# Performance work log

Measured on AMD Instinct MI355X. Metric: run time of the kernel, lower is better.

The kernel has to match this reference:

```python
import jax, jax.numpy as jnp
import numpy as np

B, T, C = 2, 2048, 2048
H, HKV, DH = 32, 8, 64
G = H // HKV  # kv_group_size = 4


def setup_inputs() -> dict:
    key = jax.random.key(0)
    k1, k2, k3, k4 = jax.random.split(key, 4)
    x = jax.random.normal(k1, (B, T, C), dtype=jnp.float32)
    Wq = jax.random.normal(k2, (C, C), dtype=jnp.float32) * 0.02
    Wkv = jax.random.normal(k3, (2 * HKV * DH, C), dtype=jnp.float32) * 0.02
    Wo = jax.random.normal(k4, (C, C), dtype=jnp.float32) * 0.02
    # RoPE tables: cos/sin of shape (T, DH/2)
    inv_freq = 1.0 / (10000.0 ** (jnp.arange(0, DH // 2, dtype=jnp.float32) / (DH // 2)))
    ang = jnp.arange(T, dtype=jnp.float32)[:, None] * inv_freq[None, :]  # (T, DH/2)
    return {"x": x, "cos": jnp.cos(ang), "sin": jnp.sin(ang), "Wq": Wq, "Wkv": Wkv, "Wo": Wo}


def _rotate_half(t):
    t1, t2 = jnp.split(t, 2, axis=-1)
    return jnp.concatenate([-t2, t1], axis=-1)


def reference(x, cos, sin, Wq, Wkv, Wo):
    # Projections (torch Linear: y = x @ W.T)
    q = (x @ Wq.T).reshape(B, T, H, DH).transpose(0, 2, 1, 3)      # (B,H,T,DH)
    kv = (x @ Wkv.T).reshape(B, T, 2, HKV, DH)
    k = kv[:, :, 0].transpose(0, 2, 1, 3)                          # (B,HKV,T,DH)
    v = kv[:, :, 1].transpose(0, 2, 1, 3)
    # RoPE
    cos2 = jnp.concatenate([cos, cos], axis=-1)[None, None]        # (1,1,T,DH)
    sin2 = jnp.concatenate([sin, sin], axis=-1)[None, None]
    q = q * cos2 + _rotate_half(q) * sin2
    k = k * cos2 + _rotate_half(k) * sin2
    # Grouped-query attention without materializing repeated K/V:
    # view q as (B, HKV, G, T, DH) and contract against shared K/V heads.
    qg = q.reshape(B, HKV, G, T, DH)
    scale = 1.0 / jnp.sqrt(jnp.float32(DH))
    scores = jnp.einsum("bhgqd,bhkd->bhgqk", qg, k) * scale        # (B,HKV,G,T,T)
    causal = jnp.tril(jnp.ones((T, T), dtype=bool))
    scores = jnp.where(causal[None, None, None], scores, -jnp.inf)
    attn = jax.nn.softmax(scores, axis=-1)
    out = jnp.einsum("bhgqk,bhkd->bhgqd", attn, v)                 # (B,HKV,G,T,DH)
    out = out.reshape(B, H, T, DH).transpose(0, 2, 1, 3).reshape(B, T, C)
    return out @ Wo.T
```

## Files before the change

kernel.cpp:

```cpp
#include <hip/hip_runtime.h>
#include <hip/hip_bf16.h>

#define B_    2
#define T_    2048
#define C_    2048
#define H_    32
#define HKV_  8
#define DH_   64
#define NQKV  3072
#define KOFF  2048
#define VOFF  2560

typedef __attribute__((ext_vector_type(4))) float f32x4;
typedef __attribute__((ext_vector_type(16))) float f32x16;
typedef __attribute__((ext_vector_type(8))) short bf16x8;
typedef __attribute__((ext_vector_type(4))) short s16x4;

__device__ __forceinline__ float bf2f(short s) {
  union { unsigned u; float f; } v; v.u = ((unsigned)(unsigned short)s) << 16; return v.f;
}
__device__ __forceinline__ short f2bf(float f) {
  union { float f; unsigned u; } v; v.f = f;
  unsigned u = v.u + 0x7fffu + ((v.u >> 16) & 1u);
  return (short)(u >> 16);
}
__device__ __forceinline__ unsigned pk2(float lo, float hi) {
  union { __hip_bfloat162 b; unsigned u; } c;
  c.b = __float22bfloat162_rn(make_float2(lo, hi));
  return c.u;
}

__device__ __forceinline__ void gload_lds16(const void* g, void* l) {
  __builtin_amdgcn_global_load_lds((const __attribute__((address_space(1))) void*)g,
                                   (__attribute__((address_space(3))) void*)l, 16, 0, 0);
}

__global__ void cvt_kernel(const float* __restrict__ src, short* __restrict__ dst, int n4) {
  int i = blockIdx.x * 256 + threadIdx.x;
  if (i >= n4) return;
  const float4 v = reinterpret_cast<const float4*>(src)[i];
  s16x4 o; o[0] = f2bf(v.x); o[1] = f2bf(v.y); o[2] = f2bf(v.z); o[3] = f2bf(v.w);
  reinterpret_cast<s16x4*>(dst)[i] = o;
}

__global__ void rope_kernel(short* __restrict__ qkv, const float* __restrict__ cosT,
                            const float* __restrict__ sinT) {
  const int r = blockIdx.y;
  const int p = blockIdx.x * 256 + threadIdx.x;
  const int t = r & (T_ - 1);
  const int dd = p & 31;
  int col0; float sc;
  if (p < 1024) { int hh = p >> 5; col0 = hh * 64 + dd; sc = 0.18033688011112042f; }
  else          { int hh = (p - 1024) >> 5; col0 = KOFF + hh * 64 + dd; sc = 1.0f; }
  const float c = cosT[t * 32 + dd], s = sinT[t * 32 + dd];
  short* base = qkv + (size_t)r * NQKV;
  const float x1 = bf2f(base[col0]);
  const float x2 = bf2f(base[col0 + 32]);
  base[col0]      = f2bf((x1 * c - x2 * s) * sc);
  base[col0 + 32] = f2bf((x2 * c + x1 * s) * sc);
}

__global__ void vtrans_kernel(const short* __restrict__ qkv, short* __restrict__ vT) {
  __shared__ short tile[64][72];
  const int tid = threadIdx.x;
  const int tt = blockIdx.x, bh = blockIdx.y;
  const int b = bh >> 3, hk = bh & 7;
#pragma unroll
  for (int i = 0; i < 2; ++i) {
    int c = tid + i * 256;
    int r = c >> 3, s = c & 7;
    bf16x8 v = *reinterpret_cast<const bf16x8*>(
        qkv + ((size_t)(b * T_ + tt * 64 + r)) * NQKV + VOFF + hk * 64 + s * 8);
#pragma unroll
    for (int e = 0; e < 8; ++e) tile[s * 8 + e][r] = v[e];
  }
  __syncthreads();
#pragma unroll
  for (int i = 0; i < 2; ++i) {
    int c = tid + i * 256;
    int d = c >> 3, s = c & 7;
    bf16x8 o;
#pragma unroll
    for (int e = 0; e < 8; ++e) o[e] = tile[d][s * 8 + e];
    *reinterpret_cast<bf16x8*>(vT + ((size_t)bh * 64 + d) * T_ + tt * 64 + s * 8) = o;
  }
}

template <int OUT_BF16>
__global__ __launch_bounds__(256) void gemm_bt(const short* __restrict__ A,
                                               const short* __restrict__ Bm,
                                               void* __restrict__ Cm,
                                               int M, int N, int K) {
  __shared__ __attribute__((aligned(16))) short Alds[128 * 32];
  __shared__ __attribute__((aligned(16))) short Blds[128 * 32];
  const int tid = threadIdx.x;
  const int w = tid >> 6, lane = tid & 63, g = lane >> 4, l15 = lane & 15;
  const int wm = (w >> 1) * 64, wn = (w & 1) * 64;

  int bid = blockIdx.y * gridDim.x + blockIdx.x;
  const int nwg = gridDim.x * gridDim.y;
  int wg = (nwg & 7) ? bid : ((bid & 7) * (nwg >> 3) + (bid >> 3));
  const int m0 = (wg / gridDim.x) * 128, n0 = (wg % gridDim.x) * 128;

  f32x4 acc[4][4] = {};

  for (int k0 = 0; k0 < K; k0 += 32) {
#pragma unroll
    for (int i = 0; i < 2; ++i) {
      int c = w * 128 + i * 64 + lane;
      int row = c >> 2, slot = c & 3;
      int ks = slot ^ ((row >> 1) & 3);
      gload_lds16(A + (size_t)(m0 + row) * K + k0 + ks * 8,
                  Alds + (w * 128 + i * 64) * 8);
      gload_lds16(Bm + (size_t)(n0 + row) * K + k0 + ks * 8,
                  Blds + (w * 128 + i * 64) * 8);
    }
    __syncthreads();
    bf16x8 af[4], bf[4];
#pragma unroll
    for (int mi = 0; mi < 4; ++mi) {
      int ra = wm + mi * 16 + l15;
      af[mi] = *reinterpret_cast<const bf16x8*>(Alds + ra * 32 + (g ^ ((ra >> 1) & 3)) * 8);
      int rb = wn + mi * 16 + l15;
      bf[mi] = *reinterpret_cast<const bf16x8*>(Blds + rb * 32 + (g ^ ((rb >> 1) & 3)) * 8);
    }
#pragma unroll
    for (int mi = 0; mi < 4; ++mi)
#pragma unroll
      for (int ni = 0; ni < 4; ++ni)
        acc[mi][ni] = __builtin_amdgcn_mfma_f32_16x16x32_bf16(af[mi], bf[ni], acc[mi][ni], 0, 0, 0);
    __syncthreads();
  }

#pragma unroll
  for (int mi = 0; mi < 4; ++mi)
#pragma unroll
    for (int ni = 0; ni < 4; ++ni) {
      const int m = m0 + wm + mi * 16 + g * 4;
      const int n = n0 + wn + ni * 16 + l15;
      if (OUT_BF16) {
        short* Cp = (short*)Cm;
#pragma unroll
        for (int r = 0; r < 4; ++r) Cp[(size_t)(m + r) * N + n] = f2bf(acc[mi][ni][r]);
      } else {
        float* Cp = (float*)Cm;
#pragma unroll
        for (int r = 0; r < 4; ++r) Cp[(size_t)(m + r) * N + n] = acc[mi][ni][r];
      }
    }
}

__global__ __launch_bounds__(256) void attn_kernel(const short* __restrict__ qkv,
                                                   const short* __restrict__ vT,
                                                   short* __restrict__ out) {
  __shared__ __attribute__((aligned(16))) short Klds[2][64 * 64];
  __shared__ __attribute__((aligned(16))) short Vlds[2][64 * 64];

  const int tid = threadIdx.x, w = tid >> 6, lane = tid & 63;
  const int l31 = lane & 31, hl = lane >> 5;

  const int bid = blockIdx.y * gridDim.x + blockIdx.x;
  const int wg = (bid & 7) * 128 + (bid >> 3);
  const int p = wg & 15, qh = wg >> 4;
  const int b = qh >> 5, h = qh & 31, hk = h >> 2;

  const int wtile = w >> 1, wq = w & 1;
  const int qt = wtile ? p : (31 - p);
  const int nt = 32 - p;
  const int myend = wtile ? (p + 1) : nt;
  const size_t browbase = (size_t)b * T_;
  const size_t qrow = browbase + qt * 64 + wq * 32 + l31;

  bf16x8 qf[4];
#pragma unroll
  for (int s = 0; s < 4; ++s)
    qf[s] = *reinterpret_cast<const bf16x8*>(qkv + qrow * NQKV + h * 64 + s * 16 + hl * 8);

  const short* kg = qkv + browbase * NQKV + KOFF + hk * 64;
  const short* vg = vT + ((size_t)(b * HKV_ + hk)) * 64 * T_;

  float m_run = -1e30f, l_run = 0.f;
  f32x16 o0 = {}, o1 = {};

  auto STAGE = [&](int kt, int buf) {
    const int kv0 = kt * 64;
#pragma unroll
    for (int i = 0; i < 2; ++i) {
      const int c = w * 128 + i * 64 + lane;
      const int j = c >> 3, slot = c & 7;
      gload_lds16(kg + (size_t)(kv0 + j) * NQKV + (slot ^ (j & 7)) * 8,
                  &Klds[buf][(w * 128 + i * 64) * 8]);
      gload_lds16(vg + (size_t)j * T_ + kv0 + (slot ^ (j & 7)) * 8,
                  &Vlds[buf][(w * 128 + i * 64) * 8]);
    }
  };

#define KFRAG(TAU, S) (*reinterpret_cast<const bf16x8*>( \
    Kc + ((TAU) * 32 + l31) * 64 + (((hl + 2 * (S)) ^ (l31 & 7)) * 8)))
#define VFRAG(DT, S) (*reinterpret_cast<const bf16x8*>( \
    Vc + ((DT) * 32 + l31) * 64 + (((hl + 2 * (S)) ^ (l31 & 7)) * 8)))

  STAGE(0, 0);
  __syncthreads();

  for (int t = 0; t < nt; ++t) {
    const int cur = t & 1;
    if (t + 1 < nt) STAGE(t + 1, cur ^ 1);
    const short* Kc = &Klds[cur][0];
    const short* Vc = &Vlds[cur][0];

    if (t < myend) {
      f32x16 st0 = {}, st1 = {};
#pragma unroll
      for (int s = 0; s < 4; ++s) {
        st0 = __builtin_amdgcn_mfma_f32_32x32x16_bf16(KFRAG(0, s), qf[s], st0, 0, 0, 0);
        st1 = __builtin_amdgcn_mfma_f32_32x32x16_bf16(KFRAG(1, s), qf[s], st1, 0, 0, 0);
      }

      if (t == myend - 1) {
        const int qq = wq * 32 + l31;
#pragma unroll
        for (int r = 0; r < 16; ++r) {
          const int j0 = (r & 3) + 8 * (r >> 2) + 4 * hl;
          if (j0 > qq)      st0[r] = -1e30f;
          if (j0 + 32 > qq) st1[r] = -1e30f;
        }
      }

      float tmax = -1e30f;
#pragma unroll
      for (int r = 0; r < 16; ++r) tmax = fmaxf(tmax, fmaxf(st0[r], st1[r]));
      tmax = fmaxf(tmax, __shfl_xor(tmax, 32));
      if (__any(tmax > m_run + 8.0f)) {
        const float m_new = fmaxf(m_run, tmax);
        const float corr = exp2f(m_run - m_new);
        l_run *= corr;
#pragma unroll
        for (int r = 0; r < 16; ++r) { o0[r] *= corr; o1[r] *= corr; }
        m_run = m_new;
      }
      float tsum = 0.f;
#pragma unroll
      for (int r = 0; r < 16; ++r) {
        st0[r] = exp2f(st0[r] - m_run); tsum += st0[r];
        st1[r] = exp2f(st1[r] - m_run); tsum += st1[r];
      }
      tsum += __shfl_xor(tsum, 32);
      l_run += tsum;

      unsigned u0[8], u1[8];
#pragma unroll
      for (int k = 0; k < 8; ++k) {
        u0[k] = pk2(st0[2 * k], st0[2 * k + 1]);
        u1[k] = pk2(st1[2 * k], st1[2 * k + 1]);
      }

#define PV_STEP(S, UU)                                                        \
      {                                                                       \
        const int base_ = ((S) & 1) * 4;                                      \
        unsigned x0 = UU[base_ + 0], y0 = UU[base_ + 2];                      \
        unsigned x1 = UU[base_ + 1], y1 = UU[base_ + 3];                      \
        asm volatile("v_permlane32_swap_b32 %0, %1" : "+v"(x0), "+v"(y0));    \
        asm volatile("v_permlane32_swap_b32 %0, %1" : "+v"(x1), "+v"(y1));    \
        union { unsigned uw[4]; bf16x8 v8; } fr_;                             \
        fr_.uw[0] = x0; fr_.uw[1] = x1; fr_.uw[2] = y0; fr_.uw[3] = y1;       \
        o0 = __builtin_amdgcn_mfma_f32_32x32x16_bf16(VFRAG(0, S), fr_.v8, o0, 0, 0, 0); \
        o1 = __builtin_amdgcn_mfma_f32_32x32x16_bf16(VFRAG(1, S), fr_.v8, o1, 0, 0, 0); \
      }
      PV_STEP(0, u0)
      PV_STEP(1, u0)
      PV_STEP(2, u1)
      PV_STEP(3, u1)
#undef PV_STEP
    }
    __syncthreads();
  }

  const float inv = 1.0f / l_run;
  short* obase = out + qrow * C_ + h * 64;
  {
#pragma unroll
    for (int rr = 0; rr < 4; ++rr) {
      s16x4 ov;
#pragma unroll
      for (int e = 0; e < 4; ++e) ov[e] = f2bf(o0[rr * 4 + e] * inv);
      *reinterpret_cast<s16x4*>(obase + rr * 8 + hl * 4) = ov;
    }
#pragma unroll
    for (int rr = 0; rr < 4; ++rr) {
      s16x4 ov;
#pragma unroll
      for (int e = 0; e < 4; ++e) ov[e] = f2bf(o1[rr * 4 + e] * inv);
      *reinterpret_cast<s16x4*>(obase + 32 + rr * 8 + hl * 4) = ov;
    }
  }
#undef KFRAG
#undef VFRAG
}

extern "C" void kernel_launch(void* const* d_in, const int* in_sizes, int n_in,
                              void* d_out, int out_size, void* d_ws, size_t ws_size,
                              hipStream_t stream) {
  const float* x    = (const float*)d_in[0];
  const float* cosT = (const float*)d_in[1];
  const float* sinT = (const float*)d_in[2];
  const float* Wq   = (const float*)d_in[3];
  const float* Wkv  = (const float*)d_in[4];
  const float* Wo   = (const float*)d_in[5];

  short* xb   = (short*)d_ws;
  short* wqkv = xb + (size_t)4096 * 2048;
  short* wob  = wqkv + (size_t)3072 * 2048;
  short* qkv  = wob + (size_t)2048 * 2048;
  short* aout = qkv + (size_t)4096 * 3072;
  short* vTb  = xb;

  cvt_kernel<<<8192, 256, 0, stream>>>(x, xb, 2097152);
  cvt_kernel<<<4096, 256, 0, stream>>>(Wq, wqkv, 1048576);
  cvt_kernel<<<2048, 256, 0, stream>>>(Wkv, wqkv + (size_t)2048 * 2048, 524288);
  cvt_kernel<<<4096, 256, 0, stream>>>(Wo, wob, 1048576);

  gemm_bt<1><<<dim3(24, 32), 256, 0, stream>>>(xb, wqkv, qkv, 4096, 3072, 2048);
  rope_kernel<<<dim3(5, 4096), 256, 0, stream>>>(qkv, cosT, sinT);
  vtrans_kernel<<<dim3(32, 16), 256, 0, stream>>>(qkv, vTb);
  attn_kernel<<<dim3(16, 64), 256, 0, stream>>>(qkv, vTb, aout);
  gemm_bt<0><<<dim3(16, 32), 256, 0, stream>>>(aout, wob, (float*)d_out, 4096, 2048, 2048);
}
```

Baseline: 392.4 us.

## Remap attention blocks to contiguous 128-row query tiles and fuse conversion launches

The attention kernel drops the paired-tile scheme, where each block handled a short and a long 64-row tile for causal balance. Each block now processes one contiguous 128-row query tile with four waves sharing the K/V stream. Blocks are assigned per XCD so heads group on the same XCD, and the launch order interleaves long and short tiles for load balance. The four fp32-to-bf16 conversion launches are merged into one kernel, which removes launch overhead but adds a branch per thread.

Result: faster. 341.2 us (-13.1%).

```diff
diff --git a/kernel.cpp b/kernel.cpp
--- a/kernel.cpp
+++ b/kernel.cpp
@@ -35,12 +35,18 @@
                                    (__attribute__((address_space(3))) void*)l, 16, 0, 0);
 }
 
-__global__ void cvt_kernel(const float* __restrict__ src, short* __restrict__ dst, int n4) {
-  int i = blockIdx.x * 256 + threadIdx.x;
-  if (i >= n4) return;
-  const float4 v = reinterpret_cast<const float4*>(src)[i];
+__global__ void cvt4_kernel(const float* __restrict__ x, const float* __restrict__ Wq,
+                            const float* __restrict__ Wkv, const float* __restrict__ Wo,
+                            short* __restrict__ dst) {
+  const int g = blockIdx.x * 256 + threadIdx.x;
+  const float* src; int off;
+  if (g < 2097152)      { src = x;   off = g; }
+  else if (g < 3145728) { src = Wq;  off = g - 2097152; }
+  else if (g < 3670016) { src = Wkv; off = g - 3145728; }
+  else                  { src = Wo;  off = g - 3670016; }
+  const float4 v = reinterpret_cast<const float4*>(src)[off];
   s16x4 o; o[0] = f2bf(v.x); o[1] = f2bf(v.y); o[2] = f2bf(v.z); o[3] = f2bf(v.w);
-  reinterpret_cast<s16x4*>(dst)[i] = o;
+  reinterpret_cast<s16x4*>(dst)[g] = o;
 }
 
 __global__ void rope_kernel(short* __restrict__ qkv, const float* __restrict__ cosT,
@@ -159,17 +165,18 @@
   const int tid = threadIdx.x, w = tid >> 6, lane = tid & 63;
   const int l31 = lane & 31, hl = lane >> 5;
 
-  const int bid = blockIdx.y * gridDim.x + blockIdx.x;
-  const int wg = (bid & 7) * 128 + (bid >> 3);
-  const int p = wg & 15, qh = wg >> 4;
+  const int bid = blockIdx.x;
+  const int xcd = bid & 7, k = bid >> 3;
+  const int qh = xcd * 8 + (k & 7);
+  const int qi = k >> 3;
+  const int m_ = qi & 3, d_ = qi >> 2;
+  const int qt = (d_ & 1) ? (2 * m_ + (d_ >> 1)) : (15 - (d_ >> 1) - 2 * m_);
   const int b = qh >> 5, h = qh & 31, hk = h >> 2;
 
-  const int wtile = w >> 1, wq = w & 1;
-  const int qt = wtile ? p : (31 - p);
-  const int nt = 32 - p;
-  const int myend = wtile ? (p + 1) : nt;
+  const int nt = 2 * qt + 2;
+  const int myend = 2 * qt + (w >> 1) + 1;
   const size_t browbase = (size_t)b * T_;
-  const size_t qrow = browbase + qt * 64 + wq * 32 + l31;
+  const size_t qrow = browbase + qt * 128 + w * 32 + l31;
 
   bf16x8 qf[4];
 #pragma unroll
@@ -218,12 +225,12 @@
       }
 
       if (t == myend - 1) {
-        const int qq = wq * 32 + l31;
+        const int dq = ((w & 1) << 5) + l31;
 #pragma unroll
         for (int r = 0; r < 16; ++r) {
           const int j0 = (r & 3) + 8 * (r >> 2) + 4 * hl;
-          if (j0 > qq)      st0[r] = -1e30f;
-          if (j0 + 32 > qq) st1[r] = -1e30f;
+          if (j0 > dq)      st0[r] = -1e30f;
+          if (j0 + 32 > dq) st1[r] = -1e30f;
         }
       }
 
@@ -250,9 +257,9 @@
 
       unsigned u0[8], u1[8];
 #pragma unroll
-      for (int k = 0; k < 8; ++k) {
-        u0[k] = pk2(st0[2 * k], st0[2 * k + 1]);
-        u1[k] = pk2(st1[2 * k], st1[2 * k + 1]);
+      for (int kk = 0; kk < 8; ++kk) {
+        u0[kk] = pk2(st0[2 * kk], st0[2 * kk + 1]);
+        u1[kk] = pk2(st1[2 * kk], st1[2 * kk + 1]);
       }
 
 #define PV_STEP(S, UU)                                                        \
@@ -278,21 +285,19 @@
 
   const float inv = 1.0f / l_run;
   short* obase = out + qrow * C_ + h * 64;
-  {
-#pragma unroll
-    for (int rr = 0; rr < 4; ++rr) {
-      s16x4 ov;
-#pragma unroll
-      for (int e = 0; e < 4; ++e) ov[e] = f2bf(o0[rr * 4 + e] * inv);
-      *reinterpret_cast<s16x4*>(obase + rr * 8 + hl * 4) = ov;
-    }
-#pragma unroll
-    for (int rr = 0; rr < 4; ++rr) {
-      s16x4 ov;
-#pragma unroll
-      for (int e = 0; e < 4; ++e) ov[e] = f2bf(o1[rr * 4 + e] * inv);
-      *reinterpret_cast<s16x4*>(obase + 32 + rr * 8 + hl * 4) = ov;
-    }
+#pragma unroll
+  for (int rr = 0; rr < 4; ++rr) {
+    s16x4 ov;
+#pragma unroll
+    for (int e = 0; e < 4; ++e) ov[e] = f2bf(o0[rr * 4 + e] * inv);
+    *reinterpret_cast<s16x4*>(obase + rr * 8 + hl * 4) = ov;
+  }
+#pragma unroll
+  for (int rr = 0; rr < 4; ++rr) {
+    s16x4 ov;
+#pragma unroll
+    for (int e = 0; e < 4; ++e) ov[e] = f2bf(o1[rr * 4 + e] * inv);
+    *reinterpret_cast<s16x4*>(obase + 32 + rr * 8 + hl * 4) = ov;
   }
 #undef KFRAG
 #undef VFRAG
@@ -315,14 +320,11 @@
   short* aout = qkv + (size_t)4096 * 3072;
   short* vTb  = xb;
 
-  cvt_kernel<<<8192, 256, 0, stream>>>(x, xb, 2097152);
-  cvt_kernel<<<4096, 256, 0, stream>>>(Wq, wqkv, 1048576);
-  cvt_kernel<<<2048, 256, 0, stream>>>(Wkv, wqkv + (size_t)2048 * 2048, 524288);
-  cvt_kernel<<<4096, 256, 0, stream>>>(Wo, wob, 1048576);
+  cvt4_kernel<<<18432, 256, 0, stream>>>(x, Wq, Wkv, Wo, (short*)d_ws);
 
   gemm_bt<1><<<dim3(24, 32), 256, 0, stream>>>(xb, wqkv, qkv, 4096, 3072, 2048);
   rope_kernel<<<dim3(5, 4096), 256, 0, stream>>>(qkv, cosT, sinT);
   vtrans_kernel<<<dim3(32, 16), 256, 0, stream>>>(qkv, vTb);
-  attn_kernel<<<dim3(16, 64), 256, 0, stream>>>(qkv, vTb, aout);
+  attn_kernel<<<1024, 256, 0, stream>>>(qkv, vTb, aout);
   gemm_bt<0><<<dim3(16, 32), 256, 0, stream>>>(aout, wob, (float*)d_out, 4096, 2048, 2048);
 }
```
